# Optimization experiments

Measured on AMD Instinct MI355X. Metric: run time of the kernel, lower is better.

Reference implementation:

```python
import jax, jax.numpy as jnp
import numpy as np

B, S, DMODEL, HEADS = 2, 2048, 1024, 16
DK = DMODEL // HEADS
DV = DMODEL // HEADS


def setup_inputs() -> dict:
    key = jax.random.key(0)
    kx, kq, kk, kv = jax.random.split(key, 4)
    x = jax.random.normal(kx, (B, S, DMODEL), dtype=jnp.float32)
    # stacked per-head projection weights, shape [H, dmodel, dk/dv]
    # (equivalent to nn.Linear(dmodel, dk, bias=False) per head)
    scale = 1.0 / np.sqrt(DMODEL)
    Wq = jax.random.uniform(kq, (HEADS, DMODEL, DK), jnp.float32, -scale, scale)
    Wk = jax.random.uniform(kk, (HEADS, DMODEL, DK), jnp.float32, -scale, scale)
    Wv = jax.random.uniform(kv, (HEADS, DMODEL, DV), jnp.float32, -scale, scale)
    return {"x": x, "Wq": Wq, "Wk": Wk, "Wv": Wv}


def reference(x, Wq, Wk, Wv):
    # per-head projections, batched across heads: [B,H,S,dk]
    q = jnp.einsum("bsd,hdk->bhsk", x, Wq)
    k = jnp.einsum("bsd,hdk->bhsk", x, Wk)
    v = jnp.einsum("bsd,hdv->bhsv", x, Wv)
    # NOTE: original module applies NO 1/sqrt(dk) scaling — keep faithful
    scores = jnp.einsum("bhqk,bhsk->bhqs", q, k)  # [B,H,S,S]
    attn = jax.nn.softmax(scores, axis=-1)
    out = jnp.einsum("bhqs,bhsv->bhqv", attn, v)  # [B,H,S,dv]
    # concat heads along last dim in head order
    Bsz, H, Sq, Dv = out.shape
    return jnp.transpose(out, (0, 2, 1, 3)).reshape(Bsz, Sq, H * Dv)
```

## Files before the change

kernel.cpp:

```cpp
#include <hip/hip_runtime.h>

#define B_ 2
#define S_ 2048
#define D_ 1024
#define H_ 16
#define DK_ 64
#define M_ (B_ * S_)
#define N_ (3 * D_)

typedef __bf16 bf16x8 __attribute__((ext_vector_type(8)));
typedef short s8vec __attribute__((ext_vector_type(8)));
typedef float f4vec __attribute__((ext_vector_type(4)));
typedef float f16vec __attribute__((ext_vector_type(16)));

static __device__ __forceinline__ ushort f2b(float f) {
  union { float f; unsigned u; } v; v.f = f;
  unsigned u = v.u;
  u += 0x7FFFu + ((u >> 16) & 1u);
  return (ushort)(u >> 16);
}

static __device__ __forceinline__ unsigned pk2(float a, float b) {
#if __has_builtin(__builtin_amdgcn_cvt_pk_bf16_f32)
  typedef __bf16 b2 __attribute__((ext_vector_type(2)));
  b2 r = __builtin_amdgcn_cvt_pk_bf16_f32(a, b);
  return __builtin_bit_cast(unsigned, r);
#else
  return (unsigned)f2b(a) | ((unsigned)f2b(b) << 16);
#endif
}

static __device__ __forceinline__ float exp2f_fast(float x) {
#if __has_builtin(__builtin_amdgcn_exp2f)
  return __builtin_amdgcn_exp2f(x);
#else
  return __expf(x * 0.6931471805599453f);
#endif
}

static __device__ __forceinline__ f4vec mfma16(s8vec a, s8vec b, f4vec c) {
  return __builtin_amdgcn_mfma_f32_16x16x32_bf16(
      __builtin_bit_cast(bf16x8, a), __builtin_bit_cast(bf16x8, b), c, 0, 0, 0);
}

static __device__ __forceinline__ f16vec mfma32(s8vec a, s8vec b, f16vec c) {
  return __builtin_amdgcn_mfma_f32_32x32x16_bf16(
      __builtin_bit_cast(bf16x8, a), __builtin_bit_cast(bf16x8, b), c, 0, 0, 0);
}

static __device__ __forceinline__ void gl_lds16(const ushort* g, ushort* l) {
  __builtin_amdgcn_global_load_lds(
      (const __attribute__((address_space(1))) unsigned*)g,
      (__attribute__((address_space(3))) unsigned*)l, 16, 0, 0);
}

static __device__ __forceinline__ void wg_barrier_lds() {
  asm volatile("" ::: "memory");
  __builtin_amdgcn_s_waitcnt(0xC07F);
  __builtin_amdgcn_s_barrier();
  asm volatile("" ::: "memory");
}

__global__ __launch_bounds__(256) void cvt_xw(const float* __restrict__ x,
                                              const float* __restrict__ Wq,
                                              const float* __restrict__ Wk,
                                              const float* __restrict__ Wv,
                                              ushort* __restrict__ xb,
                                              ushort* __restrict__ wbt) {
  __shared__ ushort T[64 * 72];
  const int t = threadIdx.x;
  if (blockIdx.x < 4096) {
    int i = blockIdx.x * 256 + t;
    float4 v = ((const float4*)x)[i];
    ushort4 o;
    o.x = f2b(v.x); o.y = f2b(v.y); o.z = f2b(v.z); o.w = f2b(v.w);
    ((ushort4*)xb)[i] = o;
    return;
  }
  const int r = blockIdx.x - 4096;
  const int w = r >> 8, h = (r >> 4) & 15, d0 = (r & 15) * 64;
  const float* W = (w == 0) ? Wq : (w == 1) ? Wk : Wv;
  const float sc = (w == 0) ? 1.4426950408889634f : 1.0f;
  const float* src = W + (size_t)h * 65536 + (size_t)d0 * 64;
#pragma unroll
  for (int j = 0; j < 4; ++j) {
    int idx = j * 256 + t;
    int dr = idx >> 4, kc = (idx & 15) * 4;
    float4 v = *(const float4*)(src + dr * 64 + kc);
    T[(kc + 0) * 72 + dr] = f2b(v.x * sc);
    T[(kc + 1) * 72 + dr] = f2b(v.y * sc);
    T[(kc + 2) * 72 + dr] = f2b(v.z * sc);
    T[(kc + 3) * 72 + dr] = f2b(v.w * sc);
  }
  __syncthreads();
  const int kk = t >> 2, dcg = (t & 3) * 16;
  ushort* dst = wbt + ((size_t)w * 1024 + h * 64 + kk) * 1024 + d0 + dcg;
  *(s8vec*)dst       = *(const s8vec*)&T[kk * 72 + dcg];
  *(s8vec*)(dst + 8) = *(const s8vec*)&T[kk * 72 + dcg + 8];
}

__global__ __launch_bounds__(512) void proj_gemm(const ushort* __restrict__ xb,
                                                 const ushort* __restrict__ wbt,
                                                 ushort* __restrict__ qkv) {
  __shared__ __attribute__((aligned(16))) ushort As[2][256 * 64];
  __shared__ __attribute__((aligned(16))) ushort Bs[2][192 * 64];
  const int tid = threadIdx.x, wid = tid >> 6, lane = tid & 63;
  const int quad = lane >> 4, l15 = lane & 15;
  const int wm = wid & 1, wn = wid >> 1;
  const int m0 = blockIdx.x * 256, n0 = blockIdx.y * 192;

  f4vec acc[8][3];
#pragma unroll
  for (int mb = 0; mb < 8; mb++)
#pragma unroll
    for (int nb = 0; nb < 3; nb++)
#pragma unroll
      for (int i = 0; i < 4; i++) acc[mb][nb][i] = 0.f;

  const int sr = tid >> 3, sg = tid & 7;
  const int gk = sg ^ (sr & 7) ^ ((sr >> 3) & 7);
  const ushort* Ab = xb + (size_t)m0 * D_;
  const ushort* Bb = wbt + (size_t)n0 * D_;

#define PSTAGE(buf, k0_)                                                    \
  do {                                                                      \
    _Pragma("unroll")                                                       \
    for (int j = 0; j < 4; ++j)                                             \
      gl_lds16(Ab + (size_t)(j * 64 + sr) * D_ + (k0_) + gk * 8,            \
               &As[buf][(j * 64 + wid * 8) * 64]);                          \
    _Pragma("unroll")                                                       \
    for (int j = 0; j < 3; ++j)                                             \
      gl_lds16(Bb + (size_t)(j * 64 + sr) * D_ + (k0_) + gk * 8,            \
               &Bs[buf][(j * 64 + wid * 8) * 64]);                          \
  } while (0)

#define PCOMP(buf)                                                          \
  do {                                                                      \
    _Pragma("unroll")                                                       \
    for (int kb = 0; kb < 2; ++kb) {                                        \
      s8vec af[8], bf[3];                                                   \
      _Pragma("unroll")                                                     \
      for (int mb = 0; mb < 8; ++mb) {                                      \
        int m = wm * 128 + mb * 16 + l15;                                   \
        int gpos = (kb * 4 + quad) ^ (m & 7) ^ ((mb * 2 + (l15 >> 3)) & 7); \
        af[mb] = *(const s8vec*)&As[buf][m * 64 + gpos * 8];                \
      }                                                                     \
      _Pragma("unroll")                                                     \
      for (int nb = 0; nb < 3; ++nb) {                                      \
        int n = wn * 48 + nb * 16 + l15;                                    \
        int gpos = (kb * 4 + quad) ^ (n & 7) ^                              \
                   ((wn * 6 + nb * 2 + (l15 >> 3)) & 7);                    \
        bf[nb] = *(const s8vec*)&Bs[buf][n * 64 + gpos * 8];                \
      }                                                                     \
      _Pragma("unroll")                                                     \
      for (int mb = 0; mb < 8; ++mb)                                        \
        _Pragma("unroll")                                                   \
        for (int nb = 0; nb < 3; ++nb)                                      \
          acc[mb][nb] = mfma16(af[mb], bf[nb], acc[mb][nb]);                \
    }                                                                       \
  } while (0)

  PSTAGE(0, 0);
  for (int t = 0; t < 15; ++t) {
    const int cur = t & 1;
    PSTAGE(cur ^ 1, (t + 1) * 64);
    asm volatile("" ::: "memory");
    __builtin_amdgcn_s_waitcnt(0x0F77);
    __builtin_amdgcn_s_barrier();
    asm volatile("" ::: "memory");
    PCOMP(cur);
    asm volatile("" ::: "memory");
    __builtin_amdgcn_s_barrier();
    asm volatile("" ::: "memory");
  }
  asm volatile("" ::: "memory");
  __builtin_amdgcn_s_waitcnt(0x0F70);
  __builtin_amdgcn_s_barrier();
  asm volatile("" ::: "memory");
  PCOMP(1);
#undef PSTAGE
#undef PCOMP

  const size_t per = (size_t)B_ * H_ * S_ * DK_;
  ushort* vt = qkv + 2 * per;
#pragma unroll
  for (int mb = 0; mb < 8; ++mb)
#pragma unroll
    for (int nb = 0; nb < 3; ++nb) {
      const int n1g = n0 + wn * 48 + nb * 16 + l15;
      const int w = n1g >> 10, n1 = n1g & 1023;
      if (w == 2) {
#pragma unroll
        for (int i = 0; i < 4; ++i) {
          int m = m0 + wm * 128 + mb * 16 + quad * 4 + i;
          int b = m >> 11, s = m & 2047;
          vt[((size_t)b * 1024 + n1) * S_ + s] = f2b(acc[mb][nb][i]);
        }
      } else {
#pragma unroll
        for (int i = 0; i < 4; ++i) {
          int m = m0 + wm * 128 + mb * 16 + quad * 4 + i;
          int b = m >> 11, s = m & 2047;
          qkv[(size_t)w * per + (((size_t)b * H_ + (n1 >> 6)) * S_ + s) * 64 + (n1 & 63)] =
              f2b(acc[mb][nb][i]);
        }
      }
    }
}

__global__ __launch_bounds__(512) void attn(const ushort* __restrict__ qg,
                                            const ushort* __restrict__ kg,
                                            const ushort* __restrict__ vtg,
                                            float* __restrict__ out) {
  __shared__ __attribute__((aligned(16))) ushort KV[128 * 64 + 2 * 64 * 64];
  __shared__ float LM[4][64];
  ushort* Ks  = KV;
  ushort* Vt0 = KV + 128 * 64;
  float*  OM  = (float*)KV;

  const int L = blockIdx.x + (blockIdx.y << 3);
  const int orig = (L & 7) * 32 + (L >> 3);
  const int qt = orig & 7, bh = orig >> 3;
  const int b = bh >> 4, h = bh & 15;
  const int tid = threadIdx.x, wid = tid >> 6, lane = tid & 63;
  const int l31 = lane & 31, hi = lane >> 5, l7 = lane & 7;
  const int qgi = wid >> 1, kh = wid & 1;

  const ushort* qb = qg + ((size_t)bh * S_ + qt * 256 + qgi * 64) * DK_;
  s8vec bq[2][4];
#pragma unroll
  for (int qs = 0; qs < 2; ++qs)
#pragma unroll
    for (int s = 0; s < 4; ++s)
      bq[qs][s] = *(const s8vec*)(qb + (size_t)(qs * 32 + l31) * DK_ + s * 16 + hi * 8);

  f16vec o[2][2];
  float lsum[2] = {0.f, 0.f};
#pragma unroll
  for (int dvh = 0; dvh < 2; ++dvh)
#pragma unroll
    for (int qs = 0; qs < 2; ++qs)
#pragma unroll
      for (int i = 0; i < 16; ++i) o[dvh][qs][i] = 0.f;

  const int r6 = tid >> 3, gs = tid & 7;
  const int gk = gs ^ (r6 & 7);
  const ushort* kb_ = kg + (size_t)bh * S_ * DK_;
  const ushort* vb_ = vtg + (size_t)bh * 64 * S_ + (size_t)r6 * S_;

  s8vec kr[2], vr[2];
  kr[0] = *(const s8vec*)(kb_ + (size_t)r6 * DK_ + gk * 8);
  kr[1] = *(const s8vec*)(kb_ + (size_t)(64 + r6) * DK_ + gk * 8);
  vr[0] = *(const s8vec*)(vb_ + gk * 8);
  vr[1] = *(const s8vec*)(vb_ + 64 + gk * 8);

  for (int kt = 0; kt < S_ / 128; ++kt) {
    wg_barrier_lds();
    *(s8vec*)&Ks[r6 * 64 + gs * 8]        = kr[0];
    *(s8vec*)&Ks[(64 + r6) * 64 + gs * 8] = kr[1];
    *(s8vec*)&Vt0[r6 * 64 + gs * 8]       = vr[0];
    *(s8vec*)&Vt0[4096 + r6 * 64 + gs * 8] = vr[1];
    if (kt + 1 < S_ / 128) {
      const ushort* kn = kb_ + (size_t)(kt + 1) * 128 * DK_;
      kr[0] = *(const s8vec*)(kn + (size_t)r6 * DK_ + gk * 8);
      kr[1] = *(const s8vec*)(kn + (size_t)(64 + r6) * DK_ + gk * 8);
      const ushort* vn = vb_ + (kt + 1) * 128;
      vr[0] = *(const s8vec*)(vn + gk * 8);
      vr[1] = *(const s8vec*)(vn + 64 + gk * 8);
    }
    wg_barrier_lds();

#pragma unroll
    for (int c = 0; c < 2; ++c) {
      const int row0 = kh * 64 + c * 32 + l31;
      s8vec ak[4];
#pragma unroll
      for (int s = 0; s < 4; ++s)
        ak[s] = *(const s8vec*)&Ks[row0 * 64 + (((2 * s + hi)) ^ l7) * 8];

      f16vec st[2];
#pragma unroll
      for (int qs = 0; qs < 2; ++qs)
#pragma unroll
        for (int i = 0; i < 16; ++i) st[qs][i] = 0.f;
#pragma unroll
      for (int s = 0; s < 4; ++s) {
        st[0] = mfma32(ak[s], bq[0][s], st[0]);
        st[1] = mfma32(ak[s], bq[1][s], st[1]);
      }

#pragma unroll
      for (int qs = 0; qs < 2; ++qs) {
        float p[16];
#pragma unroll
        for (int r = 0; r < 16; ++r) p[r] = exp2f_fast(st[qs][r]);
        float s0 = ((p[0] + p[1]) + (p[2] + p[3])) + ((p[4] + p[5]) + (p[6] + p[7]));
        float s1 = ((p[8] + p[9]) + (p[10] + p[11])) + ((p[12] + p[13]) + (p[14] + p[15]));
        lsum[qs] += s0 + s1;
#pragma unroll
        for (int m = 0; m < 2; ++m) {
          unsigned u01 = pk2(p[m * 8 + 0], p[m * 8 + 1]);
          unsigned u23 = pk2(p[m * 8 + 2], p[m * 8 + 3]);
          unsigned u89 = pk2(p[m * 8 + 4], p[m * 8 + 5]);
          unsigned uAB = pk2(p[m * 8 + 6], p[m * 8 + 7]);
          asm("v_permlane32_swap_b32 %0, %1" : "+v"(u01), "+v"(u89));
          asm("v_permlane32_swap_b32 %0, %1" : "+v"(u23), "+v"(uAB));
          union { unsigned u[4]; s8vec v; } pb;
          pb.u[0] = u01;
          pb.u[1] = u23;
          pb.u[2] = u89;
          pb.u[3] = uAB;
#pragma unroll
          for (int dvh = 0; dvh < 2; ++dvh) {
            s8vec av = *(const s8vec*)&Vt0[kh * 4096 + (dvh * 32 + l31) * 64 +
                                           ((4 * c + 2 * m + hi) ^ l7) * 8];
            o[dvh][qs] = mfma32(av, pb.v, o[dvh][qs]);
          }
        }
      }
    }
  }

#pragma unroll
  for (int qs = 0; qs < 2; ++qs) lsum[qs] += __shfl_xor(lsum[qs], 32, 64);

  __syncthreads();
#pragma unroll
  for (int rnd = 0; rnd < 2; ++rnd) {
    if (kh == 1 && (qgi >> 1) == rnd) {
      const int slot = (qgi & 1) * 4;
#pragma unroll
      for (int dvh = 0; dvh < 2; ++dvh)
#pragma unroll
        for (int qs = 0; qs < 2; ++qs)
#pragma unroll
          for (int r = 0; r < 16; ++r)
            OM[(slot + dvh * 2 + qs) * 1024 + r * 64 + lane] = o[dvh][qs][r];
      if (!hi) {
        LM[qgi][l31]      = lsum[0];
        LM[qgi][32 + l31] = lsum[1];
      }
    }
    __syncthreads();
    if (kh == 0 && (qgi >> 1) == rnd) {
      const int slot = (qgi & 1) * 4;
      float linv[2];
#pragma unroll
      for (int qs = 0; qs < 2; ++qs)
        linv[qs] = 1.0f / (lsum[qs] + LM[qgi][qs * 32 + l31]);
      float* ob = out + ((size_t)b * S_ + qt * 256 + qgi * 64) * D_ + h * DK_;
#pragma unroll
      for (int dvh = 0; dvh < 2; ++dvh)
#pragma unroll
        for (int qs = 0; qs < 2; ++qs)
#pragma unroll
          for (int qd = 0; qd < 4; ++qd) {
            float4 vv;
            vv.x = (o[dvh][qs][qd * 4 + 0] +
                    OM[(slot + dvh * 2 + qs) * 1024 + (qd * 4 + 0) * 64 + lane]) * linv[qs];
            vv.y = (o[dvh][qs][qd * 4 + 1] +
                    OM[(slot + dvh * 2 + qs) * 1024 + (qd * 4 + 1) * 64 + lane]) * linv[qs];
            vv.z = (o[dvh][qs][qd * 4 + 2] +
                    OM[(slot + dvh * 2 + qs) * 1024 + (qd * 4 + 2) * 64 + lane]) * linv[qs];
            vv.w = (o[dvh][qs][qd * 4 + 3] +
                    OM[(slot + dvh * 2 + qs) * 1024 + (qd * 4 + 3) * 64 + lane]) * linv[qs];
            *(float4*)&ob[(size_t)(qs * 32 + l31) * D_ + dvh * 32 + qd * 8 + 4 * hi] = vv;
          }
    }
    __syncthreads();
  }
}

extern "C" void kernel_launch(void* const* d_in, const int* in_sizes, int n_in,
                              void* d_out, int out_size, void* d_ws, size_t ws_size,
                              hipStream_t stream) {
  const float* x  = (const float*)d_in[0];
  const float* Wq = (const float*)d_in[1];
  const float* Wk = (const float*)d_in[2];
  const float* Wv = (const float*)d_in[3];
  float* out = (float*)d_out;

  ushort* xb  = (ushort*)d_ws;
  ushort* wbt = xb + (size_t)B_ * S_ * D_;
  ushort* qkv = wbt + (size_t)3 * D_ * D_;
  const size_t per = (size_t)B_ * H_ * S_ * DK_;

  cvt_xw<<<4096 + 768, 256, 0, stream>>>(x, Wq, Wk, Wv, xb, wbt);
  proj_gemm<<<dim3(M_ / 256, N_ / 192), 512, 0, stream>>>(xb, wbt, qkv);
  attn<<<dim3(S_ / 256, B_ * H_), 512, 0, stream>>>(qkv, qkv + per, qkv + 2 * per, out);
}
```

Before: 157.7 us.

## Double-buffer K/V tiles in LDS and merge epilogue reduction into one round

The attention kernel now keeps two LDS buffers for K and V^T tiles. Each iteration writes the next tile into the idle buffer while computing on the current one, which cuts the two barriers per iteration down to one. With the larger shared pool, the cross-wave output reduction fits in a single round instead of two serialized rounds. The cost is double the LDS use (about 64KB), which may reduce occupancy, plus a deeper register prefetch.

Result: no change. 156.7 us (-0.6%).

```diff
diff --git a/kernel.cpp b/kernel.cpp
--- a/kernel.cpp
+++ b/kernel.cpp
@@ -212,11 +212,9 @@
                                             const ushort* __restrict__ kg,
                                             const ushort* __restrict__ vtg,
                                             float* __restrict__ out) {
-  __shared__ __attribute__((aligned(16))) ushort KV[128 * 64 + 2 * 64 * 64];
+  __shared__ __attribute__((aligned(16))) ushort POOL[2][128 * 64 + 2 * 64 * 64];
   __shared__ float LM[4][64];
-  ushort* Ks  = KV;
-  ushort* Vt0 = KV + 128 * 64;
-  float*  OM  = (float*)KV;
+  float* OM = (float*)POOL;
 
   const int L = blockIdx.x + (blockIdx.y << 3);
   const int orig = (L & 7) * 32 + (L >> 3);
@@ -253,30 +251,49 @@
   kr[1] = *(const s8vec*)(kb_ + (size_t)(64 + r6) * DK_ + gk * 8);
   vr[0] = *(const s8vec*)(vb_ + gk * 8);
   vr[1] = *(const s8vec*)(vb_ + 64 + gk * 8);
+  {
+    ushort* Ksb = POOL[0];
+    ushort* Vtb = POOL[0] + 8192;
+    *(s8vec*)&Ksb[r6 * 64 + gs * 8]         = kr[0];
+    *(s8vec*)&Ksb[(64 + r6) * 64 + gs * 8]  = kr[1];
+    *(s8vec*)&Vtb[r6 * 64 + gs * 8]         = vr[0];
+    *(s8vec*)&Vtb[4096 + r6 * 64 + gs * 8]  = vr[1];
+    const ushort* kn = kb_ + (size_t)128 * DK_;
+    kr[0] = *(const s8vec*)(kn + (size_t)r6 * DK_ + gk * 8);
+    kr[1] = *(const s8vec*)(kn + (size_t)(64 + r6) * DK_ + gk * 8);
+    vr[0] = *(const s8vec*)(vb_ + 128 + gk * 8);
+    vr[1] = *(const s8vec*)(vb_ + 128 + 64 + gk * 8);
+  }
+  wg_barrier_lds();
 
   for (int kt = 0; kt < S_ / 128; ++kt) {
-    wg_barrier_lds();
-    *(s8vec*)&Ks[r6 * 64 + gs * 8]        = kr[0];
-    *(s8vec*)&Ks[(64 + r6) * 64 + gs * 8] = kr[1];
-    *(s8vec*)&Vt0[r6 * 64 + gs * 8]       = vr[0];
-    *(s8vec*)&Vt0[4096 + r6 * 64 + gs * 8] = vr[1];
+    const int cur = kt & 1;
     if (kt + 1 < S_ / 128) {
-      const ushort* kn = kb_ + (size_t)(kt + 1) * 128 * DK_;
-      kr[0] = *(const s8vec*)(kn + (size_t)r6 * DK_ + gk * 8);
-      kr[1] = *(const s8vec*)(kn + (size_t)(64 + r6) * DK_ + gk * 8);
-      const ushort* vn = vb_ + (kt + 1) * 128;
-      vr[0] = *(const s8vec*)(vn + gk * 8);
-      vr[1] = *(const s8vec*)(vn + 64 + gk * 8);
+      ushort* Ksb = POOL[cur ^ 1];
+      ushort* Vtb = POOL[cur ^ 1] + 8192;
+      *(s8vec*)&Ksb[r6 * 64 + gs * 8]         = kr[0];
+      *(s8vec*)&Ksb[(64 + r6) * 64 + gs * 8]  = kr[1];
+      *(s8vec*)&Vtb[r6 * 64 + gs * 8]         = vr[0];
+      *(s8vec*)&Vtb[4096 + r6 * 64 + gs * 8]  = vr[1];
+      if (kt + 2 < S_ / 128) {
+        const ushort* kn = kb_ + (size_t)(kt + 2) * 128 * DK_;
+        kr[0] = *(const s8vec*)(kn + (size_t)r6 * DK_ + gk * 8);
+        kr[1] = *(const s8vec*)(kn + (size_t)(64 + r6) * DK_ + gk * 8);
+        const ushort* vn = vb_ + (kt + 2) * 128;
+        vr[0] = *(const s8vec*)(vn + gk * 8);
+        vr[1] = *(const s8vec*)(vn + 64 + gk * 8);
+      }
     }
-    wg_barrier_lds();
-
+
+    const ushort* ksb = POOL[cur];
+    const ushort* vtb = POOL[cur] + 8192;
 #pragma unroll
     for (int c = 0; c < 2; ++c) {
       const int row0 = kh * 64 + c * 32 + l31;
       s8vec ak[4];
 #pragma unroll
       for (int s = 0; s < 4; ++s)
-        ak[s] = *(const s8vec*)&Ks[row0 * 64 + (((2 * s + hi)) ^ l7) * 8];
+        ak[s] = *(const s8vec*)&ksb[row0 * 64 + (((2 * s + hi)) ^ l7) * 8];
 
       f16vec st[2];
 #pragma unroll
@@ -312,62 +329,53 @@
           pb.u[3] = uAB;
 #pragma unroll
           for (int dvh = 0; dvh < 2; ++dvh) {
-            s8vec av = *(const s8vec*)&Vt0[kh * 4096 + (dvh * 32 + l31) * 64 +
+            s8vec av = *(const s8vec*)&vtb[kh * 4096 + (dvh * 32 + l31) * 64 +
                                            ((4 * c + 2 * m + hi) ^ l7) * 8];
             o[dvh][qs] = mfma32(av, pb.v, o[dvh][qs]);
           }
         }
       }
     }
+    wg_barrier_lds();
   }
 
 #pragma unroll
   for (int qs = 0; qs < 2; ++qs) lsum[qs] += __shfl_xor(lsum[qs], 32, 64);
 
+  if (kh == 1) {
+#pragma unroll
+    for (int dvh = 0; dvh < 2; ++dvh)
+#pragma unroll
+      for (int qs = 0; qs < 2; ++qs)
+#pragma unroll
+        for (int r = 0; r < 16; ++r)
+          OM[(qgi * 4 + dvh * 2 + qs) * 1024 + r * 64 + lane] = o[dvh][qs][r];
+    if (!hi) {
+      LM[qgi][l31]      = lsum[0];
+      LM[qgi][32 + l31] = lsum[1];
+    }
+  }
   __syncthreads();
-#pragma unroll
-  for (int rnd = 0; rnd < 2; ++rnd) {
-    if (kh == 1 && (qgi >> 1) == rnd) {
-      const int slot = (qgi & 1) * 4;
-#pragma unroll
-      for (int dvh = 0; dvh < 2; ++dvh)
-#pragma unroll
-        for (int qs = 0; qs < 2; ++qs)
-#pragma unroll
-          for (int r = 0; r < 16; ++r)
-            OM[(slot + dvh * 2 + qs) * 1024 + r * 64 + lane] = o[dvh][qs][r];
-      if (!hi) {
-        LM[qgi][l31]      = lsum[0];
-        LM[qgi][32 + l31] = lsum[1];
-      }
-    }
-    __syncthreads();
-    if (kh == 0 && (qgi >> 1) == rnd) {
-      const int slot = (qgi & 1) * 4;
-      float linv[2];
+  if (kh == 0) {
+    float linv[2];
+#pragma unroll
+    for (int qs = 0; qs < 2; ++qs)
+      linv[qs] = 1.0f / (lsum[qs] + LM[qgi][qs * 32 + l31]);
+    float* ob = out + ((size_t)b * S_ + qt * 256 + qgi * 64) * D_ + h * DK_;
+#pragma unroll
+    for (int dvh = 0; dvh < 2; ++dvh)
 #pragma unroll
       for (int qs = 0; qs < 2; ++qs)
-        linv[qs] = 1.0f / (lsum[qs] + LM[qgi][qs * 32 + l31]);
-      float* ob = out + ((size_t)b * S_ + qt * 256 + qgi * 64) * D_ + h * DK_;
-#pragma unroll
-      for (int dvh = 0; dvh < 2; ++dvh)
-#pragma unroll
-        for (int qs = 0; qs < 2; ++qs)
-#pragma unroll
-          for (int qd = 0; qd < 4; ++qd) {
-            float4 vv;
-            vv.x = (o[dvh][qs][qd * 4 + 0] +
-                    OM[(slot + dvh * 2 + qs) * 1024 + (qd * 4 + 0) * 64 + lane]) * linv[qs];
-            vv.y = (o[dvh][qs][qd * 4 + 1] +
-                    OM[(slot + dvh * 2 + qs) * 1024 + (qd * 4 + 1) * 64 + lane]) * linv[qs];
-            vv.z = (o[dvh][qs][qd * 4 + 2] +
-                    OM[(slot + dvh * 2 + qs) * 1024 + (qd * 4 + 2) * 64 + lane]) * linv[qs];
-            vv.w = (o[dvh][qs][qd * 4 + 3] +
-                    OM[(slot + dvh * 2 + qs) * 1024 + (qd * 4 + 3) * 64 + lane]) * linv[qs];
-            *(float4*)&ob[(size_t)(qs * 32 + l31) * D_ + dvh * 32 + qd * 8 + 4 * hi] = vv;
-          }
-    }
-    __syncthreads();
+#pragma unroll
+        for (int qd = 0; qd < 4; ++qd) {
+          const int slot = (qgi * 4 + dvh * 2 + qs) * 1024;
+          float4 vv;
+          vv.x = (o[dvh][qs][qd * 4 + 0] + OM[slot + (qd * 4 + 0) * 64 + lane]) * linv[qs];
+          vv.y = (o[dvh][qs][qd * 4 + 1] + OM[slot + (qd * 4 + 1) * 64 + lane]) * linv[qs];
+          vv.z = (o[dvh][qs][qd * 4 + 2] + OM[slot + (qd * 4 + 2) * 64 + lane]) * linv[qs];
+          vv.w = (o[dvh][qs][qd * 4 + 3] + OM[slot + (qd * 4 + 3) * 64 + lane]) * linv[qs];
+          *(float4*)&ob[(size_t)(qs * 32 + l31) * D_ + dvh * 32 + qd * 8 + 4 * hi] = vv;
+        }
   }
 }
 
```
